# Optimization experiments

Hardware: AMD Instinct MI355X
Metric: run time of the kernel (lower is better)

Reference implementation:

```python
import jax, jax.numpy as jnp
import numpy as np

POOL_SIZE = 8
SEG_LEN = 100
N_CODEBOOKS = 4
VOCAB = 1024
EMB = 128
HID = 512
LAT = 256
NUM_CODES = 1024
BETA = 0.1
BATCH = 128


def _pool_matrix(T, P):
    # torch adaptive_avg_pool1d bin boundaries
    starts = np.floor(np.arange(P) * T / P).astype(int)
    ends = np.ceil((np.arange(P) + 1) * T / P).astype(int)
    M = np.zeros((T, P), np.float32)
    for i in range(P):
        M[starts[i]:ends[i], i] = 1.0 / (ends[i] - starts[i])
    return jnp.asarray(M)

_POOL = _pool_matrix(SEG_LEN, POOL_SIZE)


def _conv1d_same3(x, w, b):
    # x: (B, Cin, T), w: (Cout, Cin, 3), padding=1
    y = jax.lax.conv_general_dilated(x, w, (1,), [(1, 1)],
                                     dimension_numbers=('NCH', 'OIH', 'NCH'))
    return y + b[None, :, None]


def _encode(tokens, emb, c1w, c1b, c2w, c2b, c3w, c3b):
    # tokens: (B, T, C) int -> z_e (B, POOL_SIZE, LAT)
    B, T, C = tokens.shape
    x = emb[tokens]                      # (B, T, C, EMB)
    x = x.reshape(B, T, C * EMB).transpose(0, 2, 1)  # (B, C*EMB, T)
    x = jax.nn.relu(_conv1d_same3(x, c1w, c1b))
    x = jax.nn.relu(_conv1d_same3(x, c2w, c2b))
    x = jnp.einsum('bct,tp->bcp', x, _POOL)          # adaptive avg pool -> (B, HID, 8)
    x = jnp.einsum('bcp,oc->bpo', x, c3w[:, :, 0]) + c3b  # 1x1 conv -> (B, 8, LAT)
    return x


def _vq(z_e, codebook):
    # z_e: (B, L, D); eval-mode EMA quantizer (no buffer update)
    cb_sq = jnp.sum(codebook ** 2, axis=-1)          # (K,)
    dist = (jnp.sum(z_e ** 2, axis=-1, keepdims=True)
            - 2.0 * jnp.einsum('bld,kd->blk', z_e, codebook) + cb_sq)
    codes = jnp.argmin(dist, axis=-1)                # (B, L)
    z_q = codebook[codes]                            # gather (B, L, D)
    z_q_st = z_e + jax.lax.stop_gradient(z_q - z_e)
    commit = jnp.mean((z_e - jax.lax.stop_gradient(z_q)) ** 2)
    return z_q_st, codes, BETA * commit


def _decode(z_prev, z_curr, z_next, fc1w, fc1b, fc2w, fc2b, d1w, d1b, d2w, d2b):
    B = z_curr.shape[0]
    z = jnp.concatenate([z_prev, z_curr, z_next], axis=1).reshape(B, -1)  # (B, 3*8*LAT)
    h = jax.nn.relu(z @ fc1w.T + fc1b)
    h = jax.nn.relu(h @ fc2w.T + fc2b)               # (B, HID)
    h = jnp.broadcast_to(h[:, :, None], (B, HID, SEG_LEN))
    # ConvTranspose1d(k=3, pad=1, stride=1) == conv with flipped, transposed kernel
    w1 = jnp.flip(jnp.swapaxes(d1w, 0, 1), -1)       # (O, I, 3)
    h = jax.nn.relu(_conv1d_same3(h, w1, d1b))
    out = jnp.einsum('bct,cv->bvt', h, d2w[:, :, 0]) + d2b[None, :, None]  # (B, V*C, T)
    logits = out.reshape(B, N_CODEBOOKS, VOCAB, SEG_LEN).transpose(0, 3, 1, 2)
    return logits                                    # (B, T, C, V)


def _model(tokens_prev, tokens_curr, tokens_next, emb, conv1_w, conv1_b,
           conv2_w, conv2_b, conv3_w, conv3_b, codebook, fc1_w, fc1_b,
           fc2_w, fc2_b, deconv1_w, deconv1_b, deconv2_w, deconv2_b):
    enc = lambda t: _encode(t, emb, conv1_w, conv1_b, conv2_w, conv2_b, conv3_w, conv3_b)
    z_prev, _, vq_prev = _vq(enc(tokens_prev), codebook)
    z_curr, _, vq_curr = _vq(enc(tokens_curr), codebook)
    z_next, _, vq_next = _vq(enc(tokens_next), codebook)
    logits = _decode(z_prev, z_curr, z_next, fc1_w, fc1_b, fc2_w, fc2_b,
                     deconv1_w, deconv1_b, deconv2_w, deconv2_b)
    logp = jax.nn.log_softmax(logits, axis=-1)
    nll = -jnp.take_along_axis(logp, tokens_curr[..., None], axis=-1)[..., 0]
    recon_loss = jnp.mean(nll)
    vq_loss = vq_prev + vq_curr + vq_next
    centered = codebook - jnp.mean(codebook, axis=0, keepdims=True)
    diversity_loss = -jnp.mean(centered ** 2)
    total = recon_loss + vq_loss + 0.0 * diversity_loss  # variance_loss_scale=0.0
    return total


def setup_inputs() -> dict:
    key = jax.random.key(0)
    ks = jax.random.split(key, 20)
    s = 0.02
    n = lambda k, shape, sc=0.02: sc * jax.random.normal(k, shape, dtype=jnp.float32)
    return {
        'tokens_prev': jax.random.randint(ks[0], (BATCH, SEG_LEN, N_CODEBOOKS), 0, VOCAB),
        'tokens_curr': jax.random.randint(ks[1], (BATCH, SEG_LEN, N_CODEBOOKS), 0, VOCAB),
        'tokens_next': jax.random.randint(ks[2], (BATCH, SEG_LEN, N_CODEBOOKS), 0, VOCAB),
        'emb': n(ks[3], (VOCAB, EMB), 1.0),
        'conv1_w': n(ks[4], (HID, EMB * N_CODEBOOKS, 3)),
        'conv1_b': jnp.zeros((HID,), jnp.float32),
        'conv2_w': n(ks[5], (HID, HID, 3)),
        'conv2_b': jnp.zeros((HID,), jnp.float32),
        'conv3_w': n(ks[6], (LAT, HID, 1)),
        'conv3_b': jnp.zeros((LAT,), jnp.float32),
        'codebook': n(ks[7], (NUM_CODES, LAT), 1.0),
        'fc1_w': n(ks[8], (HID, LAT * POOL_SIZE * 3)),
        'fc1_b': jnp.zeros((HID,), jnp.float32),
        'fc2_w': n(ks[9], (HID, HID)),
        'fc2_b': jnp.zeros((HID,), jnp.float32),
        'deconv1_w': n(ks[10], (HID, HID, 3)),
        'deconv1_b': jnp.zeros((HID,), jnp.float32),
        'deconv2_w': n(ks[11], (HID, VOCAB * N_CODEBOOKS, 1)),
        'deconv2_b': jnp.zeros((VOCAB * N_CODEBOOKS,), jnp.float32),
    }


def reference(tokens_prev, tokens_curr, tokens_next, emb, conv1_w, conv1_b,
              conv2_w, conv2_b, conv3_w, conv3_b, codebook, fc1_w, fc1_b,
              fc2_w, fc2_b, deconv1_w, deconv1_b, deconv2_w, deconv2_b):
    return _model(tokens_prev, tokens_curr, tokens_next, emb, conv1_w, conv1_b,
                  conv2_w, conv2_b, conv3_w, conv3_b, codebook, fc1_w, fc1_b,
                  fc2_w, fc2_b, deconv1_w, deconv1_b, deconv2_w, deconv2_b)
```

## Files before the change

### kernel.cpp

```cpp
#include <hip/hip_runtime.h>
#include <math.h>

#define B_    128
#define T_    100
#define TPAD  104
#define CB_   4
#define EMB_  128
#define NROW  39936

typedef __attribute__((ext_vector_type(8))) short short8;
typedef __attribute__((ext_vector_type(4))) short short4v;
typedef __attribute__((ext_vector_type(4))) float f32x4;

__device__ __forceinline__ short f2bf(float x) {
  unsigned u = __builtin_bit_cast(unsigned, x);
  u += 0x7fffu + ((u >> 16) & 1u);
  return (short)(u >> 16);
}
__device__ __forceinline__ float bf2f(short s) {
  unsigned u = ((unsigned)(unsigned short)s) << 16;
  return __builtin_bit_cast(float, u);
}

#define GLOAD_LDS(g, l) __builtin_amdgcn_global_load_lds( \
    (const __attribute__((address_space(1))) void*)(g),   \
    (__attribute__((address_space(3))) void*)(l), 16, 0, 0)

#define MFMA16(a, b, c) __builtin_amdgcn_mfma_f32_16x16x32_bf16(a, b, c, 0, 0, 0)
#define SWZ(row, slot) (((slot) + ((row) >> 1)) & 3)

__global__ void k_prep(const float* __restrict__ c1w, const float* __restrict__ c2w,
                       const float* __restrict__ c3w, const float* __restrict__ cbk,
                       const float* __restrict__ fc1w, const float* __restrict__ fc2w,
                       const float* __restrict__ d1w, const float* __restrict__ d2w,
                       short* __restrict__ XbS, short* __restrict__ YbS,
                       short* __restrict__ Wb1, short* __restrict__ Wb2,
                       short* __restrict__ c3wB, short* __restrict__ cbkB,
                       short* __restrict__ fc1wB, short* __restrict__ fc2wB,
                       short* __restrict__ SB, short* __restrict__ d2wTB,
                       float* __restrict__ cbsq) {
  __shared__ float tile[32][33];
  int bid = blockIdx.x;
  int id = bid * 256 + threadIdx.x;
  if (bid < 24072) {
    if (id < 2048) {
      short* buf = (id >> 10) ? YbS : XbS;
      int rem = id & 1023;
      int row = rem >> 9, c = rem & 511;
      long off = row ? ((long)(NROW + 1) * 512 + c) : c;
      buf[off] = 0;
    } else if (id < 1574912) {
      int local = id - 2048;
      const float* w = (local < 786432) ? c1w : c2w;
      short* o = (local < 786432) ? Wb1 : Wb2;
      int l2 = (local < 786432) ? local : local - 786432;
      int i = l2 & 511, oo = (l2 >> 9) & 511, tap = l2 >> 18;
      o[l2] = f2bf(w[oo * 1536 + i * 3 + tap]);
    } else if (id < 1705984) {
      int l = id - 1574912;
      c3wB[l] = f2bf(c3w[l]);
    } else if (id < 1968128) {
      int l = id - 1705984;
      cbkB[l] = f2bf(cbk[l]);
    } else if (id < 5113856) {
      int l = id - 1968128;
      fc1wB[l] = f2bf(fc1w[l]);
    } else if (id < 5376000) {
      int l = id - 5113856;
      fc2wB[l] = f2bf(fc2w[l]);
    } else {
      int l = id - 5376000;
      int i = l & 511, o = (l >> 9) & 511, cls = l >> 18;
      const float* w = d1w + (i * 512 + o) * 3;
      float v;
      if (cls == 0)      v = w[0] + w[1];
      else if (cls == 1) v = w[0] + w[1] + w[2];
      else               v = w[1] + w[2];
      SB[(cls * 512 + o) * 512 + i] = f2bf(v);
    }
  } else if (bid < 26120) {
    int blk = bid - 24072;
    int bx = blk & 127, by = blk >> 7;
    int tx = threadIdx.x & 31, ty = threadIdx.x >> 5;
    #pragma unroll
    for (int j = 0; j < 32; j += 8)
      tile[ty + j][tx] = d2w[(by * 32 + ty + j) * 4096 + bx * 32 + tx];
    __syncthreads();
    #pragma unroll
    for (int j = 0; j < 32; j += 8)
      d2wTB[(bx * 32 + ty + j) * 512 + by * 32 + tx] = f2bf(tile[tx][ty + j]);
  } else {
    int idx = (bid - 26120) * 256 + threadIdx.x;
    int row = idx >> 6, lane = threadIdx.x & 63;
    float4 v = *(const float4*)&cbk[row * 256 + lane * 4];
    float s = v.x * v.x + v.y * v.y + v.z * v.z + v.w * v.w;
    #pragma unroll
    for (int m = 1; m < 64; m <<= 1) s += __shfl_xor(s, m);
    if (lane == 0) cbsq[row] = s;
  }
}

__global__ void k_embed(const int* __restrict__ t0, const int* __restrict__ t1,
                        const int* __restrict__ t2, const float* __restrict__ emb,
                        short* __restrict__ x) {
  int id = blockIdx.x * 256 + threadIdx.x;
  int c8 = id & 63;
  int row = id >> 6;
  int t = row % TPAD;
  int sb = row / TPAD;
  int b = sb & 127, s = sb >> 7;
  short8 v = {};
  if (t < T_) {
    const int* tok = (s == 0) ? t0 : (s == 1) ? t1 : t2;
    int tk = tok[(b * T_ + t) * CB_ + (c8 >> 4)];
    const float* e = emb + tk * EMB_ + (c8 & 15) * 8;
    float4 f0 = *(const float4*)e;
    float4 f1 = *(const float4*)(e + 4);
    v[0] = f2bf(f0.x); v[1] = f2bf(f0.y); v[2] = f2bf(f0.z); v[3] = f2bf(f0.w);
    v[4] = f2bf(f1.x); v[5] = f2bf(f1.y); v[6] = f2bf(f1.z); v[7] = f2bf(f1.w);
  }
  ((short8*)x)[(long)(row + 1) * 64 + c8] = v;
}

__global__ __launch_bounds__(256) void k_conv3_mfma(const short* __restrict__ X,
                                                    const short* __restrict__ Wb,
                                                    const float* __restrict__ bias,
                                                    short* __restrict__ Y) {
  __shared__ short sm[16896];
  int r0 = blockIdx.y * 128;
  int o0 = blockIdx.x * 128;
  int tid = threadIdx.x;
  int lane = tid & 63, wid = tid >> 6;
  int wm = wid >> 1, wn = wid & 1;
  int ls = lane >> 4, lr = lane & 15;
  int g = ((lane & 3) - ((lane >> 3) & 3)) & 3;
  long laneoff = (long)(lane >> 2) * 512 + g * 8;

  const short* gp[9];
  const short* lp[9];
  #pragma unroll
  for (int i = 0; i < 9; ++i) {
    int q = wid + 4 * i;
    if (q < 33) {
      long base;
      const short* src;
      if (q < 9) { src = X; base = (long)(r0 - 1 + 16 * q) * 512; }
      else {
        int b = q - 9, tap = b >> 3, j = b & 7;
        src = Wb; base = (long)(tap * 512 + o0 + 16 * j) * 512;
      }
      gp[i] = src + base + laneoff;
      lp[i] = sm + q * 512;
    }
  }

  f32x4 acc[4][4] = {};
  for (int kc = 0; kc < 512; kc += 32) {
    __syncthreads();
    #pragma unroll
    for (int i = 0; i < 9; ++i) {
      int q = wid + 4 * i;
      if (q < 33) {
        GLOAD_LDS(gp[i], lp[i]);
        gp[i] += 32;
      }
    }
    __syncthreads();
    const short8* A8 = (const short8*)sm;
    const short8* B8 = (const short8*)(sm + 4608);
    #pragma unroll
    for (int tap = 0; tap < 3; ++tap) {
      short8 a[4], b[4];
      #pragma unroll
      for (int m = 0; m < 4; ++m) {
        int row = wm * 64 + m * 16 + lr + tap;
        a[m] = A8[row * 4 + SWZ(row, ls)];
      }
      #pragma unroll
      for (int n = 0; n < 4; ++n) {
        int row = wn * 64 + n * 16 + lr;
        b[n] = B8[(tap * 128 + row) * 4 + SWZ(row, ls)];
      }
      #pragma unroll
      for (int m = 0; m < 4; ++m)
        #pragma unroll
        for (int n = 0; n < 4; ++n)
          acc[m][n] = MFMA16(a[m], b[n], acc[m][n]);
    }
  }
  #pragma unroll
  for (int m = 0; m < 4; ++m) {
    #pragma unroll
    for (int n = 0; n < 4; ++n) {
      int col = o0 + wn * 64 + n * 16 + lr;
      float bv = bias[col];
      #pragma unroll
      for (int j = 0; j < 4; ++j) {
        int r = r0 + wm * 64 + m * 16 + ls * 4 + j;
        int t = r % TPAD;
        float v = (t < T_) ? fmaxf(acc[m][n][j] + bv, 0.f) : 0.f;
        Y[(long)r * 512 + col] = f2bf(v);
      }
    }
  }
}

__global__ __launch_bounds__(256) void k_gemm_mfma(const short* __restrict__ A,
                                                   const short* __restrict__ B,
                                                   float* __restrict__ C,
                                                   short* __restrict__ Cb,
                                                   const float* __restrict__ bias,
                                                   int K, int N, int relu) {
  __shared__ short sm[8192];
  int r0 = blockIdx.x * 128;
  int o0 = blockIdx.y * 128;
  int tid = threadIdx.x;
  int lane = tid & 63, wid = tid >> 6;
  int wm = wid >> 1, wn = wid & 1;
  int ls = lane >> 4, lr = lane & 15;
  int g = ((lane & 3) - ((lane >> 3) & 3)) & 3;
  long laneoff = (long)(lane >> 2) * K + g * 8;

  const short* gp[4];
  const short* lp[4];
  #pragma unroll
  for (int i = 0; i < 4; ++i) {
    int q = wid + 4 * i;
    const short* src;
    long base;
    if (q < 8) { src = A; base = (long)(r0 + 16 * q) * K; }
    else       { src = B; base = (long)(o0 + 16 * (q - 8)) * K; }
    gp[i] = src + base + laneoff;
    lp[i] = sm + q * 512;
  }

  f32x4 acc[4][4] = {};
  for (int kc = 0; kc < K; kc += 32) {
    __syncthreads();
    #pragma unroll
    for (int i = 0; i < 4; ++i) {
      GLOAD_LDS(gp[i], lp[i]);
      gp[i] += 32;
    }
    __syncthreads();
    const short8* A8 = (const short8*)sm;
    const short8* B8 = (const short8*)(sm + 4096);
    short8 a[4], b[4];
    #pragma unroll
    for (int m = 0; m < 4; ++m) {
      int row = wm * 64 + m * 16 + lr;
      a[m] = A8[row * 4 + SWZ(row, ls)];
    }
    #pragma unroll
    for (int n = 0; n < 4; ++n) {
      int row = wn * 64 + n * 16 + lr;
      b[n] = B8[row * 4 + SWZ(row, ls)];
    }
    #pragma unroll
    for (int m = 0; m < 4; ++m)
      #pragma unroll
      for (int n = 0; n < 4; ++n)
        acc[m][n] = MFMA16(a[m], b[n], acc[m][n]);
  }
  #pragma unroll
  for (int m = 0; m < 4; ++m) {
    #pragma unroll
    for (int n = 0; n < 4; ++n) {
      int col = o0 + wn * 64 + n * 16 + lr;
      float bv = bias ? bias[col] : 0.f;
      #pragma unroll
      for (int j = 0; j < 4; ++j) {
        int r = r0 + wm * 64 + m * 16 + ls * 4 + j;
        float v = acc[m][n][j] + bv;
        if (relu) v = fmaxf(v, 0.f);
        C[(long)r * N + col] = v;
        if (Cb) Cb[(long)r * N + col] = f2bf(v);
      }
    }
  }
}

__global__ __launch_bounds__(256) void k_gemm_mfma_sk(const short* __restrict__ A,
                                                      const short* __restrict__ B,
                                                      float* __restrict__ part,
                                                      int M, int N, int K,
                                                      int kchunk, int KS, long bgstride) {
  __shared__ short sm[8192];
  int r0 = blockIdx.x * 128;
  int o0 = blockIdx.y * 128;
  int bz = blockIdx.z;
  int g = bz / KS, zz = bz - g * KS;
  const short* Bg = B + (long)g * bgstride;
  int k0 = zz * kchunk;
  int tid = threadIdx.x;
  int lane = tid & 63, wid = tid >> 6;
  int wm = wid >> 1, wn = wid & 1;
  int ls = lane >> 4, lr = lane & 15;
  int gsl = ((lane & 3) - ((lane >> 3) & 3)) & 3;
  long laneoff = (long)(lane >> 2) * K + gsl * 8 + k0;

  const short* gp[4];
  const short* lp[4];
  #pragma unroll
  for (int i = 0; i < 4; ++i) {
    int q = wid + 4 * i;
    const short* src;
    long base;
    if (q < 8) { src = A;  base = (long)(r0 + 16 * q) * K; }
    else       { src = Bg; base = (long)(o0 + 16 * (q - 8)) * K; }
    gp[i] = src + base + laneoff;
    lp[i] = sm + q * 512;
  }

  f32x4 acc[4][4] = {};
  for (int kc = 0; kc < kchunk; kc += 32) {
    __syncthreads();
    #pragma unroll
    for (int i = 0; i < 4; ++i) {
      GLOAD_LDS(gp[i], lp[i]);
      gp[i] += 32;
    }
    __syncthreads();
    const short8* A8 = (const short8*)sm;
    const short8* B8 = (const short8*)(sm + 4096);
    short8 a[4], b[4];
    #pragma unroll
    for (int m = 0; m < 4; ++m) {
      int row = wm * 64 + m * 16 + lr;
      a[m] = A8[row * 4 + SWZ(row, ls)];
    }
    #pragma unroll
    for (int n = 0; n < 4; ++n) {
      int row = wn * 64 + n * 16 + lr;
      b[n] = B8[row * 4 + SWZ(row, ls)];
    }
    #pragma unroll
    for (int m = 0; m < 4; ++m)
      #pragma unroll
      for (int n = 0; n < 4; ++n)
        acc[m][n] = MFMA16(a[m], b[n], acc[m][n]);
  }
  float* P = part + (long)bz * M * N;
  #pragma unroll
  for (int m = 0; m < 4; ++m) {
    #pragma unroll
    for (int n = 0; n < 4; ++n) {
      int col = o0 + wn * 64 + n * 16 + lr;
      #pragma unroll
      for (int j = 0; j < 4; ++j) {
        int r = r0 + wm * 64 + m * 16 + ls * 4 + j;
        P[(long)r * N + col] = acc[m][n][j];
      }
    }
  }
}

__global__ void k_reduce_bf16(const float* __restrict__ part, short* __restrict__ Cb,
                              const float* __restrict__ bias, int N, int MN,
                              int KS, int relu, int total4) {
  int id = blockIdx.x * 256 + threadIdx.x;
  if (id >= total4) return;
  int e = id * 4;
  int g = e / MN;
  int rem = e - g * MN;
  const float* base = part + (long)g * KS * MN + rem;
  float4 s = *(const float4*)base;
  for (int j = 1; j < KS; ++j) {
    float4 v = *(const float4*)(base + (long)j * MN);
    s.x += v.x; s.y += v.y; s.z += v.z; s.w += v.w;
  }
  int c = rem % N;
  s.x += bias[c]; s.y += bias[c + 1]; s.z += bias[c + 2]; s.w += bias[c + 3];
  if (relu) {
    s.x = fmaxf(s.x, 0.f); s.y = fmaxf(s.y, 0.f);
    s.z = fmaxf(s.z, 0.f); s.w = fmaxf(s.w, 0.f);
  }
  short4v o;
  o[0] = f2bf(s.x); o[1] = f2bf(s.y); o[2] = f2bf(s.z); o[3] = f2bf(s.w);
  *(short4v*)&Cb[(long)g * MN + rem] = o;
}

__global__ void k_pool(const short* __restrict__ Xg, short* __restrict__ pooledB) {
  int id = blockIdx.x * 256 + threadIdx.x;
  int row = id >> 6, cg = id & 63;
  int s = row >> 10, bp = row & 1023;
  int b = bp >> 3, p = bp & 7;
  int t0 = (p * 25) >> 1;
  const short8* src = (const short8*)(Xg + (long)((s * 128 + b) * TPAD + t0) * 512) + cg;
  float acc[8] = {};
  #pragma unroll
  for (int j = 0; j < 13; ++j) {
    short8 v = src[j * 64];
    #pragma unroll
    for (int k = 0; k < 8; ++k) acc[k] += bf2f(v[k]);
  }
  short8 o;
  #pragma unroll
  for (int k = 0; k < 8; ++k) o[k] = f2bf(acc[k] * (1.f / 13.f));
  ((short8*)pooledB)[(long)row * 64 + cg] = o;
}

__global__ __launch_bounds__(256) void k_vq(const float* __restrict__ dot,
                                            const float* __restrict__ cbsq,
                                            const float* __restrict__ ze,
                                            const float* __restrict__ cb,
                                            const short* __restrict__ cbkB,
                                            short* __restrict__ zallB,
                                            float* __restrict__ commit_part) {
  __shared__ float sv[256];
  __shared__ int si[256];
  int row = blockIdx.x, tid = threadIdx.x;
  float best = 3.4e38f; int bi = 0;
  #pragma unroll
  for (int j = 0; j < 4; ++j) {
    int k = tid * 4 + j;
    float d = cbsq[k] - 2.f * dot[(long)row * 1024 + k];
    if (d < best) { best = d; bi = k; }
  }
  sv[tid] = best; si[tid] = bi;
  __syncthreads();
  for (int off = 128; off; off >>= 1) {
    if (tid < off) {
      float o = sv[tid + off]; int oi = si[tid + off];
      if (o < sv[tid] || (o == sv[tid] && oi < si[tid])) { sv[tid] = o; si[tid] = oi; }
    }
    __syncthreads();
  }
  int ks = si[0];
  float zq = cb[ks * 256 + tid];
  float zev = ze[(long)row * 256 + tid];
  int s = row >> 10, bp = row & 1023;
  int b = bp >> 3, p = bp & 7;
  zallB[b * 6144 + s * 2048 + p * 256 + tid] = cbkB[ks * 256 + tid];
  float d = zev - zq;
  __syncthreads();
  sv[tid] = d * d;
  __syncthreads();
  for (int off = 128; off; off >>= 1) { if (tid < off) sv[tid] += sv[tid + off]; __syncthreads(); }
  if (tid == 0) commit_part[row] = sv[0];
}

__global__ __launch_bounds__(256) void k_logits_lse_recon(const float* __restrict__ part,
                                                          const float* __restrict__ d2b,
                                                          const int* __restrict__ tok,
                                                          float* __restrict__ rpart2) {
  __shared__ float row[1024];
  __shared__ float sm[256];
  int blk = blockIdx.x;
  int cb_i = blk & 3, b = (blk >> 2) & 127, cls = blk >> 9;
  int m = cls * 128 + b;
  const float* p0 = part + (long)m * 4096 + cb_i * 1024;
  const float* p1 = p0 + (long)384 * 4096;
  const float* bb = d2b + cb_i * 1024;
  int tid = threadIdx.x;
  float v[4];
  #pragma unroll
  for (int j = 0; j < 4; ++j) {
    int c = tid + 256 * j;
    v[j] = p0[c] + p1[c] + bb[c];
    row[c] = v[j];
  }
  float mx = fmaxf(fmaxf(v[0], v[1]), fmaxf(v[2], v[3]));
  sm[tid] = mx; __syncthreads();
  for (int off = 128; off; off >>= 1) { if (tid < off) sm[tid] = fmaxf(sm[tid], sm[tid + off]); __syncthreads(); }
  float gm = sm[0]; __syncthreads();
  float e = expf(v[0] - gm) + expf(v[1] - gm) + expf(v[2] - gm) + expf(v[3] - gm);
  sm[tid] = e; __syncthreads();
  for (int off = 128; off; off >>= 1) { if (tid < off) sm[tid] += sm[tid + off]; __syncthreads(); }
  float lse = gm + logf(sm[0]);
  __syncthreads();
  float val = 0.f;
  if (cls == 1) {
    if (tid < 98) {
      int tk = tok[(b * T_ + tid + 1) * CB_ + cb_i];
      val = lse - row[tk];
    }
  } else if (tid == 0) {
    int t = (cls == 0) ? 0 : 99;
    int tk = tok[(b * T_ + t) * CB_ + cb_i];
    val = lse - row[tk];
  }
  sm[tid] = val; __syncthreads();
  for (int off = 128; off; off >>= 1) { if (tid < off) sm[tid] += sm[tid + off]; __syncthreads(); }
  if (tid == 0) rpart2[blk] = sm[0];
}

__global__ void k_final(const float* __restrict__ rpart2, const float* __restrict__ cpart,
                        float* __restrict__ out) {
  __shared__ float sm[256];
  __shared__ float rs;
  int tid = threadIdx.x;
  float r = 0.f;
  #pragma unroll
  for (int j = 0; j < 6; ++j) r += rpart2[tid + 256 * j];
  sm[tid] = r; __syncthreads();
  for (int off = 128; off; off >>= 1) { if (tid < off) sm[tid] += sm[tid + off]; __syncthreads(); }
  if (tid == 0) rs = sm[0];
  __syncthreads();
  float c = 0.f;
  #pragma unroll
  for (int j = 0; j < 12; ++j) c += cpart[tid + 256 * j];
  sm[tid] = c; __syncthreads();
  for (int off = 128; off; off >>= 1) { if (tid < off) sm[tid] += sm[tid + off]; __syncthreads(); }
  if (tid == 0) out[0] = rs / 51200.f + 0.1f * (sm[0] / 262144.f);
}

extern "C" void kernel_launch(void* const* d_in, const int* in_sizes, int n_in,
                              void* d_out, int out_size, void* d_ws, size_t ws_size,
                              hipStream_t stream) {
  const int*   tok_prev = (const int*)d_in[0];
  const int*   tok_curr = (const int*)d_in[1];
  const int*   tok_next = (const int*)d_in[2];
  const float* emb  = (const float*)d_in[3];
  const float* c1w  = (const float*)d_in[4];
  const float* c1b  = (const float*)d_in[5];
  const float* c2w  = (const float*)d_in[6];
  const float* c2b  = (const float*)d_in[7];
  const float* c3w  = (const float*)d_in[8];
  const float* c3b  = (const float*)d_in[9];
  const float* cbk  = (const float*)d_in[10];
  const float* fc1w = (const float*)d_in[11];
  const float* fc1b = (const float*)d_in[12];
  const float* fc2w = (const float*)d_in[13];
  const float* fc2b = (const float*)d_in[14];
  const float* d1w  = (const float*)d_in[15];
  const float* d1b  = (const float*)d_in[16];
  const float* d2w  = (const float*)d_in[17];
  const float* d2b  = (const float*)d_in[18];

  float* ws = (float*)d_ws;
  short* XbS = (short*)ws;
  short* YbS = (short*)(ws + 10224128);
  float* fp  = ws + 2 * 10224128;
  short* Wb1    = (short*)fp;
  short* Wb2    = (short*)(fp + 393216);
  short* c3wB   = (short*)(fp + 786432);
  short* cbkB   = (short*)(fp + 851968);
  short* pooledB= (short*)(fp + 983040);
  float* ze     = fp + 1769472;
  short* zeB    = (short*)(fp + 2555904);
  short* fc1wB  = (short*)(fp + 2949120);
  short* fc2wB  = (short*)(fp + 4521984);
  short* SB     = (short*)(fp + 4653056);
  short* d2wTB  = (short*)(fp + 5046272);
  float* dotb   = fp + 6094848;
  float* cbsq   = dotb + 3145728;
  short* zallB  = (short*)(cbsq + 1024);
  float* cpart  = cbsq + 1024 + 393216;
  short* h1B    = (short*)(cpart + 3072);
  short* h2B    = (short*)(cpart + 35840);
  short* h2cB   = (short*)(cpart + 68608);
  float* rpart2 = cpart + 166912;

  const short* X = XbS + 512;
  short* Yv = YbS + 512;
  float* part = dotb;

  k_prep<<<26376, 256, 0, stream>>>(c1w, c2w, c3w, cbk, fc1w, fc2w, d1w, d2w,
                                    XbS, YbS, Wb1, Wb2, c3wB, cbkB, fc1wB, fc2wB,
                                    SB, d2wTB, cbsq);

  k_embed     <<<9984, 256, 0, stream>>>(tok_prev, tok_curr, tok_next, emb, XbS);
  k_conv3_mfma<<<dim3(4, 312), 256, 0, stream>>>(X, Wb1, c1b, Yv);
  k_conv3_mfma<<<dim3(4, 312), 256, 0, stream>>>((const short*)Yv, Wb2, c2b, (short*)X);
  k_pool      <<<768, 256, 0, stream>>>(X, pooledB);
  k_gemm_mfma <<<dim3(24, 2), 256, 0, stream>>>(pooledB, c3wB, ze, zeB, c3b, 512, 256, 0);
  k_gemm_mfma <<<dim3(24, 8), 256, 0, stream>>>(zeB, cbkB, dotb, nullptr, nullptr, 256, 1024, 0);
  k_vq        <<<3072, 256, 0, stream>>>(dotb, cbsq, ze, cbk, cbkB, zallB, cpart);

  k_gemm_mfma_sk<<<dim3(1, 4, 16), 256, 0, stream>>>(zallB, fc1wB, part, 128, 512, 6144, 384, 16, 0);
  k_reduce_bf16 <<<64, 256, 0, stream>>>(part, h1B, fc1b, 512, 65536, 16, 1, 16384);
  k_gemm_mfma_sk<<<dim3(1, 4, 8), 256, 0, stream>>>(h1B, fc2wB, part, 128, 512, 512, 64, 8, 0);
  k_reduce_bf16 <<<64, 256, 0, stream>>>(part, h2B, fc2b, 512, 65536, 8, 1, 16384);
  k_gemm_mfma_sk<<<dim3(1, 4, 24), 256, 0, stream>>>(h2B, SB, part, 128, 512, 512, 64, 8, 262144);
  k_reduce_bf16 <<<192, 256, 0, stream>>>(part, h2cB, d1b, 512, 65536, 8, 1, 49152);
  k_gemm_mfma_sk<<<dim3(3, 32, 2), 256, 0, stream>>>(h2cB, d2wTB, part, 384, 4096, 512, 256, 2, 0);
  k_logits_lse_recon<<<1536, 256, 0, stream>>>(part, d2b, tok_curr, rpart2);

  k_final<<<1, 256, 0, stream>>>(rpart2, cpart, (float*)d_out);
}
```

Baseline: 294.0 us.

## Fuse embedding gather into conv1 and argmin into codebook distance GEMM

The embedding lookup is folded into the first conv kernel: tokens are read per row and bf16 embedding rows are loaded directly into LDS, so the padded X activation buffer is no longer written and reread. The embedding table is converted to bf16 in the prep kernel, with a zero row for padding. The codebook dot-product GEMM now computes distances and per-tile argmins in its epilogue and writes 8 partial candidates per row instead of the full 3072x1024 dot matrix. A small combine kernel then picks the final code. The cost is irregular gather loads inside the conv's K loop, plus an extra reduction stage.

```diff
diff --git a/kernel.cpp b/kernel.cpp
--- a/kernel.cpp
+++ b/kernel.cpp
@@ -7,6 +7,7 @@
 #define CB_   4
 #define EMB_  128
 #define NROW  39936
+#define ZOFF  131072
 
 typedef __attribute__((ext_vector_type(8))) short short8;
 typedef __attribute__((ext_vector_type(4))) short short4v;
@@ -29,11 +30,12 @@
 #define MFMA16(a, b, c) __builtin_amdgcn_mfma_f32_16x16x32_bf16(a, b, c, 0, 0, 0)
 #define SWZ(row, slot) (((slot) + ((row) >> 1)) & 3)
 
-__global__ void k_prep(const float* __restrict__ c1w, const float* __restrict__ c2w,
+__global__ void k_prep(const float* __restrict__ emb,
+                       const float* __restrict__ c1w, const float* __restrict__ c2w,
                        const float* __restrict__ c3w, const float* __restrict__ cbk,
                        const float* __restrict__ fc1w, const float* __restrict__ fc2w,
                        const float* __restrict__ d1w, const float* __restrict__ d2w,
-                       short* __restrict__ XbS, short* __restrict__ YbS,
+                       short* __restrict__ YbS, short* __restrict__ embB,
                        short* __restrict__ Wb1, short* __restrict__ Wb2,
                        short* __restrict__ c3wB, short* __restrict__ cbkB,
                        short* __restrict__ fc1wB, short* __restrict__ fc2wB,
@@ -42,34 +44,37 @@
   __shared__ float tile[32][33];
   int bid = blockIdx.x;
   int id = bid * 256 + threadIdx.x;
-  if (bid < 24072) {
-    if (id < 2048) {
-      short* buf = (id >> 10) ? YbS : XbS;
-      int rem = id & 1023;
-      int row = rem >> 9, c = rem & 511;
+  if (bid < 24581) {
+    if (id < 1024) {
+      int row = id >> 9, c = id & 511;
       long off = row ? ((long)(NROW + 1) * 512 + c) : c;
-      buf[off] = 0;
-    } else if (id < 1574912) {
-      int local = id - 2048;
+      YbS[off] = 0;
+    } else if (id < 132096) {
+      int l = id - 1024;
+      embB[l] = f2bf(emb[l]);
+    } else if (id < 132224) {
+      embB[ZOFF + (id - 132096)] = 0;
+    } else if (id < 1705088) {
+      int local = id - 132224;
       const float* w = (local < 786432) ? c1w : c2w;
       short* o = (local < 786432) ? Wb1 : Wb2;
       int l2 = (local < 786432) ? local : local - 786432;
       int i = l2 & 511, oo = (l2 >> 9) & 511, tap = l2 >> 18;
       o[l2] = f2bf(w[oo * 1536 + i * 3 + tap]);
-    } else if (id < 1705984) {
-      int l = id - 1574912;
+    } else if (id < 1836160) {
+      int l = id - 1705088;
       c3wB[l] = f2bf(c3w[l]);
-    } else if (id < 1968128) {
-      int l = id - 1705984;
+    } else if (id < 2098304) {
+      int l = id - 1836160;
       cbkB[l] = f2bf(cbk[l]);
-    } else if (id < 5113856) {
-      int l = id - 1968128;
+    } else if (id < 5244032) {
+      int l = id - 2098304;
       fc1wB[l] = f2bf(fc1w[l]);
-    } else if (id < 5376000) {
-      int l = id - 5113856;
+    } else if (id < 5506176) {
+      int l = id - 5244032;
       fc2wB[l] = f2bf(fc2w[l]);
-    } else {
-      int l = id - 5376000;
+    } else if (id < 6292608) {
+      int l = id - 5506176;
       int i = l & 511, o = (l >> 9) & 511, cls = l >> 18;
       const float* w = d1w + (i * 512 + o) * 3;
       float v;
@@ -78,8 +83,8 @@
       else               v = w[1] + w[2];
       SB[(cls * 512 + o) * 512 + i] = f2bf(v);
     }
-  } else if (bid < 26120) {
-    int blk = bid - 24072;
+  } else if (bid < 26629) {
+    int blk = bid - 24581;
     int bx = blk & 127, by = blk >> 7;
     int tx = threadIdx.x & 31, ty = threadIdx.x >> 5;
     #pragma unroll
@@ -90,7 +95,7 @@
     for (int j = 0; j < 32; j += 8)
       d2wTB[(bx * 32 + ty + j) * 512 + by * 32 + tx] = f2bf(tile[tx][ty + j]);
   } else {
-    int idx = (bid - 26120) * 256 + threadIdx.x;
+    int idx = (bid - 26629) * 256 + threadIdx.x;
     int row = idx >> 6, lane = threadIdx.x & 63;
     float4 v = *(const float4*)&cbk[row * 256 + lane * 4];
     float s = v.x * v.x + v.y * v.y + v.z * v.z + v.w * v.w;
@@ -100,26 +105,113 @@
   }
 }
 
-__global__ void k_embed(const int* __restrict__ t0, const int* __restrict__ t1,
-                        const int* __restrict__ t2, const float* __restrict__ emb,
-                        short* __restrict__ x) {
-  int id = blockIdx.x * 256 + threadIdx.x;
-  int c8 = id & 63;
-  int row = id >> 6;
-  int t = row % TPAD;
-  int sb = row / TPAD;
-  int b = sb & 127, s = sb >> 7;
-  short8 v = {};
-  if (t < T_) {
-    const int* tok = (s == 0) ? t0 : (s == 1) ? t1 : t2;
-    int tk = tok[(b * T_ + t) * CB_ + (c8 >> 4)];
-    const float* e = emb + tk * EMB_ + (c8 & 15) * 8;
-    float4 f0 = *(const float4*)e;
-    float4 f1 = *(const float4*)(e + 4);
-    v[0] = f2bf(f0.x); v[1] = f2bf(f0.y); v[2] = f2bf(f0.z); v[3] = f2bf(f0.w);
-    v[4] = f2bf(f1.x); v[5] = f2bf(f1.y); v[6] = f2bf(f1.z); v[7] = f2bf(f1.w);
-  }
-  ((short8*)x)[(long)(row + 1) * 64 + c8] = v;
+__global__ __launch_bounds__(256) void k_conv1_embed(const int* __restrict__ tok0,
+                                                     const int* __restrict__ tok1,
+                                                     const int* __restrict__ tok2,
+                                                     const short* __restrict__ embB,
+                                                     const short* __restrict__ Wb,
+                                                     const float* __restrict__ bias,
+                                                     short* __restrict__ Y) {
+  __shared__ short sm[16896];
+  int r0 = blockIdx.y * 128;
+  int o0 = blockIdx.x * 128;
+  int tid = threadIdx.x;
+  int lane = tid & 63, wid = tid >> 6;
+  int wm = wid >> 1, wn = wid & 1;
+  int ls = lane >> 4, lr = lane & 15;
+  int g = ((lane & 3) - ((lane >> 3) & 3)) & 3;
+
+  int toff[3][4];
+  #pragma unroll
+  for (int i = 0; i < 3; ++i) {
+    int q = wid + 4 * i;
+    if (q < 9) {
+      int rr = r0 - 1 + 16 * q + (lane >> 2);
+      bool ok = (rr >= 0) && (rr < NROW);
+      int sb = ok ? (rr / 104) : 0;
+      int t = rr - sb * 104;
+      ok = ok && (t < T_);
+      int b = sb & 127, s = sb >> 7;
+      const int* tokp = (s == 0) ? tok0 : (s == 1) ? tok1 : tok2;
+      if (ok) {
+        int4 tv = *(const int4*)&tokp[(b * T_ + t) * CB_];
+        toff[i][0] = tv.x * EMB_; toff[i][1] = tv.y * EMB_;
+        toff[i][2] = tv.z * EMB_; toff[i][3] = tv.w * EMB_;
+      } else {
+        toff[i][0] = toff[i][1] = toff[i][2] = toff[i][3] = ZOFF;
+      }
+    }
+  }
+  const short* gpw[9];
+  short* lpw[9];
+  #pragma unroll
+  for (int i = 0; i < 9; ++i) {
+    int q = wid + 4 * i;
+    if (q >= 9 && q < 33) {
+      int b = q - 9, tap = b >> 3, jj = b & 7;
+      gpw[i] = Wb + (long)(tap * 512 + o0 + 16 * jj) * 512 + (long)(lane >> 2) * 512 + g * 8;
+      lpw[i] = sm + q * 512;
+    }
+  }
+
+  f32x4 acc[4][4] = {};
+  #pragma unroll
+  for (int cb = 0; cb < 4; ++cb) {
+    #pragma unroll
+    for (int kk = 0; kk < 4; ++kk) {
+      __syncthreads();
+      #pragma unroll
+      for (int i = 0; i < 3; ++i) {
+        int q = wid + 4 * i;
+        if (q < 9) GLOAD_LDS(embB + toff[i][cb] + kk * 32 + g * 8, sm + q * 512);
+      }
+      #pragma unroll
+      for (int i = 0; i < 9; ++i) {
+        int q = wid + 4 * i;
+        if (q >= 9 && q < 33) {
+          GLOAD_LDS(gpw[i], lpw[i]);
+          gpw[i] += 32;
+        }
+      }
+      __syncthreads();
+      const short8* A8 = (const short8*)sm;
+      const short8* B8 = (const short8*)(sm + 4608);
+      #pragma unroll
+      for (int tap = 0; tap < 3; ++tap) {
+        short8 a[4], b[4];
+        #pragma unroll
+        for (int m = 0; m < 4; ++m) {
+          int row = wm * 64 + m * 16 + lr + tap;
+          a[m] = A8[row * 4 + SWZ(row, ls)];
+        }
+        #pragma unroll
+        for (int n = 0; n < 4; ++n) {
+          int row = wn * 64 + n * 16 + lr;
+          b[n] = B8[(tap * 128 + row) * 4 + SWZ(row, ls)];
+        }
+        #pragma unroll
+        for (int m = 0; m < 4; ++m)
+          #pragma unroll
+          for (int n = 0; n < 4; ++n)
+            acc[m][n] = MFMA16(a[m], b[n], acc[m][n]);
+      }
+    }
+  }
+  #pragma unroll
+  for (int m = 0; m < 4; ++m) {
+    #pragma unroll
+    for (int n = 0; n < 4; ++n) {
+      int col = o0 + wn * 64 + n * 16 + lr;
+      float bv = bias[col];
+      #pragma unroll
+      for (int j = 0; j < 4; ++j) {
+        int r = r0 + wm * 64 + m * 16 + ls * 4 + j;
+        int t = r % TPAD;
+        float v = (t < T_) ? fmaxf(acc[m][n][j] + bv, 0.f) : 0.f;
+        Y[(long)r * 512 + col] = f2bf(v);
+      }
+    }
+  }
 }
 
 __global__ __launch_bounds__(256) void k_conv3_mfma(const short* __restrict__ X,
@@ -278,6 +370,136 @@
       }
     }
   }
+}
+
+__global__ __launch_bounds__(256) void k_dot_argmin(const short* __restrict__ A,
+                                                    const short* __restrict__ B,
+                                                    const float* __restrict__ cbsq,
+                                                    float* __restrict__ apv,
+                                                    int* __restrict__ api) {
+  __shared__ short sm[8192];
+  __shared__ float svv[128][2];
+  __shared__ int sii[128][2];
+  const int K = 256;
+  int r0 = blockIdx.x * 128;
+  int o0 = blockIdx.y * 128;
+  int tid = threadIdx.x;
+  int lane = tid & 63, wid = tid >> 6;
+  int wm = wid >> 1, wn = wid & 1;
+  int ls = lane >> 4, lr = lane & 15;
+  int g = ((lane & 3) - ((lane >> 3) & 3)) & 3;
+  long laneoff = (long)(lane >> 2) * K + g * 8;
+
+  const short* gp[4];
+  const short* lp[4];
+  #pragma unroll
+  for (int i = 0; i < 4; ++i) {
+    int q = wid + 4 * i;
+    const short* src;
+    long base;
+    if (q < 8) { src = A; base = (long)(r0 + 16 * q) * K; }
+    else       { src = B; base = (long)(o0 + 16 * (q - 8)) * K; }
+    gp[i] = src + base + laneoff;
+    lp[i] = sm + q * 512;
+  }
+
+  f32x4 acc[4][4] = {};
+  #pragma unroll
+  for (int kc = 0; kc < K; kc += 32) {
+    __syncthreads();
+    #pragma unroll
+    for (int i = 0; i < 4; ++i) {
+      GLOAD_LDS(gp[i], lp[i]);
+      gp[i] += 32;
+    }
+    __syncthreads();
+    const short8* A8 = (const short8*)sm;
+    const short8* B8 = (const short8*)(sm + 4096);
+    short8 a[4], b[4];
+    #pragma unroll
+    for (int m = 0; m < 4; ++m) {
+      int row = wm * 64 + m * 16 + lr;
+      a[m] = A8[row * 4 + SWZ(row, ls)];
+    }
+    #pragma unroll
+    for (int n = 0; n < 4; ++n) {
+      int row = wn * 64 + n * 16 + lr;
+      b[n] = B8[row * 4 + SWZ(row, ls)];
+    }
+    #pragma unroll
+    for (int m = 0; m < 4; ++m)
+      #pragma unroll
+      for (int n = 0; n < 4; ++n)
+        acc[m][n] = MFMA16(a[m], b[n], acc[m][n]);
+  }
+  float cq[4];
+  #pragma unroll
+  for (int n = 0; n < 4; ++n) cq[n] = cbsq[o0 + wn * 64 + n * 16 + lr];
+  #pragma unroll
+  for (int m = 0; m < 4; ++m) {
+    #pragma unroll
+    for (int j = 0; j < 4; ++j) {
+      float bv = 3.4e38f; int bi = 0x7fffffff;
+      #pragma unroll
+      for (int n = 0; n < 4; ++n) {
+        int col = o0 + wn * 64 + n * 16 + lr;
+        float v = cq[n] - 2.f * acc[m][n][j];
+        if (v < bv || (v == bv && col < bi)) { bv = v; bi = col; }
+      }
+      #pragma unroll
+      for (int d = 1; d < 16; d <<= 1) {
+        float ov = __shfl_xor(bv, d);
+        int oi = __shfl_xor(bi, d);
+        if (ov < bv || (ov == bv && oi < bi)) { bv = ov; bi = oi; }
+      }
+      if (lr == 0) {
+        int rl = wm * 64 + m * 16 + ls * 4 + j;
+        svv[rl][wn] = bv;
+        sii[rl][wn] = bi;
+      }
+    }
+  }
+  __syncthreads();
+  if (tid < 128) {
+    float v0 = svv[tid][0], v1 = svv[tid][1];
+    int i0 = sii[tid][0], i1 = sii[tid][1];
+    bool t1 = (v1 < v0) || (v1 == v0 && i1 < i0);
+    apv[(long)(r0 + tid) * 8 + blockIdx.y] = t1 ? v1 : v0;
+    api[(long)(r0 + tid) * 8 + blockIdx.y] = t1 ? i1 : i0;
+  }
+}
+
+__global__ __launch_bounds__(256) void k_vq_combine(const float* __restrict__ apv,
+                                                    const int* __restrict__ api,
+                                                    const float* __restrict__ ze,
+                                                    const float* __restrict__ cb,
+                                                    const short* __restrict__ cbkB,
+                                                    short* __restrict__ zallB,
+                                                    float* __restrict__ commit_part) {
+  __shared__ float sv[256];
+  __shared__ int ksb;
+  int row = blockIdx.x, tid = threadIdx.x;
+  if (tid == 0) {
+    float bv = apv[(long)row * 8]; int bi = api[(long)row * 8];
+    #pragma unroll
+    for (int j = 1; j < 8; ++j) {
+      float v = apv[(long)row * 8 + j]; int i = api[(long)row * 8 + j];
+      if (v < bv || (v == bv && i < bi)) { bv = v; bi = i; }
+    }
+    ksb = bi;
+  }
+  __syncthreads();
+  int ks = ksb;
+  float zq = cb[ks * 256 + tid];
+  float zev = ze[(long)row * 256 + tid];
+  int s = row >> 10, bp = row & 1023;
+  int b = bp >> 3, p = bp & 7;
+  zallB[b * 6144 + s * 2048 + p * 256 + tid] = cbkB[ks * 256 + tid];
+  float d = zev - zq;
+  sv[tid] = d * d;
+  __syncthreads();
+  for (int off = 128; off; off >>= 1) { if (tid < off) sv[tid] += sv[tid + off]; __syncthreads(); }
+  if (tid == 0) commit_part[row] = sv[0];
 }
 
 __global__ __launch_bounds__(256) void k_gemm_mfma_sk(const short* __restrict__ A,
@@ -398,46 +620,6 @@
   #pragma unroll
   for (int k = 0; k < 8; ++k) o[k] = f2bf(acc[k] * (1.f / 13.f));
   ((short8*)pooledB)[(long)row * 64 + cg] = o;
-}
-
-__global__ __launch_bounds__(256) void k_vq(const float* __restrict__ dot,
-                                            const float* __restrict__ cbsq,
-                                            const float* __restrict__ ze,
-                                            const float* __restrict__ cb,
-                                            const short* __restrict__ cbkB,
-                                            short* __restrict__ zallB,
-                                            float* __restrict__ commit_part) {
-  __shared__ float sv[256];
-  __shared__ int si[256];
-  int row = blockIdx.x, tid = threadIdx.x;
-  float best = 3.4e38f; int bi = 0;
-  #pragma unroll
-  for (int j = 0; j < 4; ++j) {
-    int k = tid * 4 + j;
-    float d = cbsq[k] - 2.f * dot[(long)row * 1024 + k];
-    if (d < best) { best = d; bi = k; }
-  }
-  sv[tid] = best; si[tid] = bi;
-  __syncthreads();
-  for (int off = 128; off; off >>= 1) {
-    if (tid < off) {
-      float o = sv[tid + off]; int oi = si[tid + off];
-      if (o < sv[tid] || (o == sv[tid] && oi < si[tid])) { sv[tid] = o; si[tid] = oi; }
-    }
-    __syncthreads();
-  }
-  int ks = si[0];
-  float zq = cb[ks * 256 + tid];
-  float zev = ze[(long)row * 256 + tid];
-  int s = row >> 10, bp = row & 1023;
-  int b = bp >> 3, p = bp & 7;
-  zallB[b * 6144 + s * 2048 + p * 256 + tid] = cbkB[ks * 256 + tid];
-  float d = zev - zq;
-  __syncthreads();
-  sv[tid] = d * d;
-  __syncthreads();
-  for (int off = 128; off; off >>= 1) { if (tid < off) sv[tid] += sv[tid + off]; __syncthreads(); }
-  if (tid == 0) commit_part[row] = sv[0];
 }
 
 __global__ __launch_bounds__(256) void k_logits_lse_recon(const float* __restrict__ part,
@@ -543,30 +725,32 @@
   short* fc2wB  = (short*)(fp + 4521984);
   short* SB     = (short*)(fp + 4653056);
   short* d2wTB  = (short*)(fp + 5046272);
-  float* dotb   = fp + 6094848;
-  float* cbsq   = dotb + 3145728;
+  float* part   = fp + 6094848;
+  float* cbsq   = part + 3145728;
   short* zallB  = (short*)(cbsq + 1024);
   float* cpart  = cbsq + 1024 + 393216;
   short* h1B    = (short*)(cpart + 3072);
   short* h2B    = (short*)(cpart + 35840);
   short* h2cB   = (short*)(cpart + 68608);
   float* rpart2 = cpart + 166912;
-
-  const short* X = XbS + 512;
-  short* Yv = YbS + 512;
-  float* part = dotb;
-
-  k_prep<<<26376, 256, 0, stream>>>(c1w, c2w, c3w, cbk, fc1w, fc2w, d1w, d2w,
-                                    XbS, YbS, Wb1, Wb2, c3wB, cbkB, fc1wB, fc2wB,
+  float* apv    = cpart + 168448;
+  int*   api    = (int*)(cpart + 193024);
+  short* embB   = (short*)(cpart + 217600);
+
+  const short* Yv = YbS + 512;
+  short* Xc = XbS + 512;
+
+  k_prep<<<26885, 256, 0, stream>>>(emb, c1w, c2w, c3w, cbk, fc1w, fc2w, d1w, d2w,
+                                    YbS, embB, Wb1, Wb2, c3wB, cbkB, fc1wB, fc2wB,
                                     SB, d2wTB, cbsq);
 
-  k_embed     <<<9984, 256, 0, stream>>>(tok_prev, tok_curr, tok_next, emb, XbS);
-  k_conv3_mfma<<<dim3(4, 312), 256, 0, stream>>>(X, Wb1, c1b, Yv);
-  k_conv3_mfma<<<dim3(4, 312), 256, 0, stream>>>((const short*)Yv, Wb2, c2b, (short*)X);
-  k_pool      <<<768, 256, 0, stream>>>(X, pooledB);
-  k_gemm_mfma <<<dim3(24, 2), 256, 0, stream>>>(pooledB, c3wB, ze, zeB, c3b, 512, 256, 0);
-  k_gemm_mfma <<<dim3(24, 8), 256, 0, stream>>>(zeB, cbkB, dotb, nullptr, nullptr, 256, 1024, 0);
-  k_vq        <<<3072, 256, 0, stream>>>(dotb, cbsq, ze, cbk, cbkB, zallB, cpart);
+  k_conv1_embed<<<dim3(4, 312), 256, 0, stream>>>(tok_prev, tok_curr, tok_next,
+                                                  embB, Wb1, c1b, (short*)Yv);
+  k_conv3_mfma <<<dim3(4, 312), 256, 0, stream>>>(Yv, Wb2, c2b, Xc);
+  k_pool       <<<768, 256, 0, stream>>>(Xc, pooledB);
+  k_gemm_mfma  <<<dim3(24, 2), 256, 0, stream>>>(pooledB, c3wB, ze, zeB, c3b, 512, 256, 0);
+  k_dot_argmin <<<dim3(24, 8), 256, 0, stream>>>(zeB, cbkB, cbsq, apv, api);
+  k_vq_combine <<<3072, 256, 0, stream>>>(apv, api, ze, cbk, cbkB, zallB, cpart);
 
   k_gemm_mfma_sk<<<dim3(1, 4, 16), 256, 0, stream>>>(zallB, fc1wB, part, 128, 512, 6144, 384, 16, 0);
   k_reduce_bf16 <<<64, 256, 0, stream>>>(part, h1B, fc1b, 512, 65536, 16, 1, 16384);
```

Result: faster. 274.5 us (-6.7%).
